# Performance work log

Hardware: AMD Instinct MI355X
Metric: run time of the kernel (lower is better)

## Reference

```python
import jax, jax.numpy as jnp
import numpy as np

PI = 3.141592653589793
L, B, D, EMAS = 4096, 16, 128, 8


def setup_inputs() -> dict:
    key = jax.random.key(0)
    x = jax.random.normal(key, (L, B, D), dtype=jnp.float32)
    # learned parameter of the EMA module: log-space decays
    log_decay = jnp.linspace(-PI, PI, EMAS, dtype=jnp.float32)
    return {"x": x, "log_decay": log_decay}


def reference(x, log_decay):
    # decay per EMA channel, in (0, 1)
    decay = jax.nn.sigmoid(log_decay)                     # [emas]
    # initial state: x[0] repeated along new emas axis
    state = jnp.broadcast_to(x[0][..., None], x[0].shape + (decay.shape[0],))  # [B, D, emas]

    def ema_step(ema_0, x_1):
        # x_1: [B, D, 1] broadcasts against decay [emas]
        ema_1 = decay * x_1 + (1.0 - decay) * ema_0
        return ema_1, ema_1

    _, ema_x = jax.lax.scan(ema_step, state, x[..., None])  # ys: [L, B, D, emas]
    return ema_x
```

## Files before the change

### kernel.cpp

```cpp
#include <hip/hip_runtime.h>


#define LL    4096
#define BB    16
#define DD    128
#define EMAS  8
#define BDSZ  (BB * DD)
#define CHUNK 32
#define HALO  128
#define NCHUNK (LL / CHUNK)
#define U     16

typedef float f32x4 __attribute__((ext_vector_type(4)));

__global__ __launch_bounds__(256) void ema_kernel(const float* __restrict__ x,
                                                  const float* __restrict__ log_decay,
                                                  float* __restrict__ out) {
    const int tid   = threadIdx.x;
    const int d     = tid & (DD - 1);
    const int bsub  = tid >> 7;
    const int bg    = blockIdx.x & 7;
    const int chunk = blockIdx.x >> 3;
    const int b     = bg * 2 + bsub;
    const int off   = b * DD + d;

    float dec[EMAS], a[EMAS];
#pragma unroll
    for (int e = 0; e < EMAS; ++e) {
        const float ld = log_decay[e];
        const float dd = 1.0f / (1.0f + __expf(-ld));
        dec[e] = dd;
        a[e]   = 1.0f - dd;
    }

    const int cstart = chunk * CHUNK;
    int l0 = cstart - HALO;
    if (l0 < 0) l0 = 0;
    const int nsteps   = (cstart - l0) + CHUNK;
    const int nblk     = nsteps / U;
    const int halo_blk = (cstart - l0) / U;

    const float* xb = x + (size_t)l0 * BDSZ + off;

    const float s0 = *xb;
    float s[EMAS];
#pragma unroll
    for (int e = 0; e < EMAS; ++e) s[e] = s0;

    f32x4* op = (f32x4*)(out + ((size_t)cstart * BDSZ + off) * EMAS);
    const int opstride = BDSZ * EMAS / 4;

#define LOADBLK(BUF, IDX)                                                      \
    do {                                                                       \
        int _i = (IDX); if (_i > nblk - 1) _i = nblk - 1;                      \
        const float* _p = xb + (size_t)_i * U * BDSZ;                          \
        _Pragma("unroll")                                                      \
        for (int u = 0; u < U; ++u) (BUF)[u] = _p[(size_t)u * BDSZ];           \
    } while (0)

#define PROCESS(BUF, J)                                                        \
    do {                                                                       \
        if ((J) >= halo_blk) {                                                 \
            _Pragma("unroll")                                                  \
            for (int u = 0; u < U; ++u) {                                      \
                const float xv = (BUF)[u];                                     \
                _Pragma("unroll")                                              \
                for (int e = 0; e < EMAS; ++e)                                 \
                    s[e] = fmaf(a[e], s[e], dec[e] * xv);                      \
                f32x4 lo = {s[0], s[1], s[2], s[3]};                           \
                f32x4 hi = {s[4], s[5], s[6], s[7]};                           \
                op[0] = lo;                                                    \
                op[1] = hi;                                                    \
                op += opstride;                                                \
            }                                                                  \
        } else {                                                               \
            _Pragma("unroll")                                                  \
            for (int u = 0; u < U; ++u) {                                      \
                const float xv = (BUF)[u];                                     \
                _Pragma("unroll")                                              \
                for (int e = 0; e < EMAS; ++e)                                 \
                    s[e] = fmaf(a[e], s[e], dec[e] * xv);                      \
            }                                                                  \
        }                                                                      \
    } while (0)

    float b0[U], b1[U], b2[U];
    LOADBLK(b0, 0);
    LOADBLK(b1, 1);

    int j = 0;
    for (; j + 2 < nblk; j += 3) {
        LOADBLK(b2, j + 2);
        PROCESS(b0, j);
        LOADBLK(b0, j + 3);
        PROCESS(b1, j + 1);
        LOADBLK(b1, j + 4);
        PROCESS(b2, j + 2);
    }
    if (j < nblk)     PROCESS(b0, j);
    if (j + 1 < nblk) PROCESS(b1, j + 1);
#undef PROCESS
#undef LOADBLK
}

extern "C" void kernel_launch(void* const* d_in, const int* in_sizes, int n_in,
                              void* d_out, int out_size, void* d_ws, size_t ws_size,
                              hipStream_t stream) {
    const float* x  = (const float*)d_in[0];
    const float* ld = (const float*)d_in[1];
    float* out      = (float*)d_out;
    (void)in_sizes; (void)n_in; (void)out_size; (void)d_ws; (void)ws_size;

    dim3 grid(NCHUNK * 8);
    dim3 block(256);
    ema_kernel<<<grid, block, 0, stream>>>(x, ld, out);
}
```

Baseline: 67.04 us.

## Prefetch chunk inputs upfront and split halo warmup from output loop

Switches to 1024-thread blocks covering half the batch-feature plane per chunk. The 32 output-step inputs are now loaded at kernel start alongside the halo prefetch, which overlaps their latency with the halo warmup. Halo processing uses smaller 8-step blocks with a separate pipelined loop, and the output phase runs without per-block branching. In exchange it raises register pressure, and the larger blocks reduce the number of workgroups.

Measured after the change: 104.6 us. +56.0%, slower.

```diff
diff --git a/kernel.cpp b/kernel.cpp
--- a/kernel.cpp
+++ b/kernel.cpp
@@ -9,20 +9,17 @@
 #define CHUNK 32
 #define HALO  128
 #define NCHUNK (LL / CHUNK)
-#define U     16
+#define U     8
 
 typedef float f32x4 __attribute__((ext_vector_type(4)));
 
-__global__ __launch_bounds__(256) void ema_kernel(const float* __restrict__ x,
-                                                  const float* __restrict__ log_decay,
-                                                  float* __restrict__ out) {
-    const int tid   = threadIdx.x;
-    const int d     = tid & (DD - 1);
-    const int bsub  = tid >> 7;
-    const int bg    = blockIdx.x & 7;
-    const int chunk = blockIdx.x >> 3;
-    const int b     = bg * 2 + bsub;
-    const int off   = b * DD + d;
+__global__ __launch_bounds__(1024) void ema_kernel(const float* __restrict__ x,
+                                                   const float* __restrict__ log_decay,
+                                                   float* __restrict__ out) {
+    const int tid  = threadIdx.x;
+    const int half = blockIdx.x & 1;
+    const int c    = blockIdx.x >> 1;
+    const int off  = (half << 10) + tid;
 
     float dec[EMAS], a[EMAS];
 #pragma unroll
@@ -33,74 +30,85 @@
         a[e]   = 1.0f - dd;
     }
 
-    const int cstart = chunk * CHUNK;
-    int l0 = cstart - HALO;
-    if (l0 < 0) l0 = 0;
-    const int nsteps   = (cstart - l0) + CHUNK;
-    const int nblk     = nsteps / U;
-    const int halo_blk = (cstart - l0) / U;
-
-    const float* xb = x + (size_t)l0 * BDSZ + off;
+    const int cstart = c * CHUNK;
+    const int front  = cstart < HALO ? cstart : HALO;
+    const int nfb    = front / U;
+    const float* xb  = x + (size_t)(cstart - front) * BDSZ + off;
 
     const float s0 = *xb;
     float s[EMAS];
 #pragma unroll
     for (int e = 0; e < EMAS; ++e) s[e] = s0;
 
-    f32x4* op = (f32x4*)(out + ((size_t)cstart * BDSZ + off) * EMAS);
-    const int opstride = BDSZ * EMAS / 4;
-
-#define LOADBLK(BUF, IDX)                                                      \
+#define LOADF(BUF, IDX)                                                        \
     do {                                                                       \
-        int _i = (IDX); if (_i > nblk - 1) _i = nblk - 1;                      \
-        const float* _p = xb + (size_t)_i * U * BDSZ;                          \
-        _Pragma("unroll")                                                      \
-        for (int u = 0; u < U; ++u) (BUF)[u] = _p[(size_t)u * BDSZ];           \
-    } while (0)
-
-#define PROCESS(BUF, J)                                                        \
-    do {                                                                       \
-        if ((J) >= halo_blk) {                                                 \
+        if ((IDX) < nfb) {                                                     \
+            const float* _p = xb + (size_t)(IDX) * U * BDSZ;                   \
             _Pragma("unroll")                                                  \
-            for (int u = 0; u < U; ++u) {                                      \
-                const float xv = (BUF)[u];                                     \
-                _Pragma("unroll")                                              \
-                for (int e = 0; e < EMAS; ++e)                                 \
-                    s[e] = fmaf(a[e], s[e], dec[e] * xv);                      \
-                f32x4 lo = {s[0], s[1], s[2], s[3]};                           \
-                f32x4 hi = {s[4], s[5], s[6], s[7]};                           \
-                op[0] = lo;                                                    \
-                op[1] = hi;                                                    \
-                op += opstride;                                                \
-            }                                                                  \
-        } else {                                                               \
-            _Pragma("unroll")                                                  \
-            for (int u = 0; u < U; ++u) {                                      \
-                const float xv = (BUF)[u];                                     \
-                _Pragma("unroll")                                              \
-                for (int e = 0; e < EMAS; ++e)                                 \
-                    s[e] = fmaf(a[e], s[e], dec[e] * xv);                      \
-            }                                                                  \
+            for (int u = 0; u < U; ++u) (BUF)[u] = _p[(size_t)u * BDSZ];       \
         }                                                                      \
     } while (0)
 
-    float b0[U], b1[U], b2[U];
-    LOADBLK(b0, 0);
-    LOADBLK(b1, 1);
+#define PROCF(BUF)                                                             \
+    do {                                                                       \
+        _Pragma("unroll")                                                      \
+        for (int u = 0; u < U; ++u) {                                          \
+            const float xv = (BUF)[u];                                         \
+            _Pragma("unroll")                                                  \
+            for (int e = 0; e < EMAS; ++e)                                     \
+                s[e] = fmaf(a[e], s[e], dec[e] * xv);                          \
+        }                                                                      \
+    } while (0)
+
+    float f0[U], f1[U], f2[U];
+    LOADF(f0, 0);
+    LOADF(f1, 1);
+
+    float c0[16], c1[16];
+    {
+        const float* xs = xb + (size_t)front * BDSZ;
+#pragma unroll
+        for (int u = 0; u < 16; ++u) c0[u] = xs[(size_t)u * BDSZ];
+#pragma unroll
+        for (int u = 0; u < 16; ++u) c1[u] = xs[(size_t)(16 + u) * BDSZ];
+    }
 
     int j = 0;
-    for (; j + 2 < nblk; j += 3) {
-        LOADBLK(b2, j + 2);
-        PROCESS(b0, j);
-        LOADBLK(b0, j + 3);
-        PROCESS(b1, j + 1);
-        LOADBLK(b1, j + 4);
-        PROCESS(b2, j + 2);
+    for (; j + 2 < nfb; j += 3) {
+        LOADF(f2, j + 2);
+        PROCF(f0);
+        LOADF(f0, j + 3);
+        PROCF(f1);
+        LOADF(f1, j + 4);
+        PROCF(f2);
     }
-    if (j < nblk)     PROCESS(b0, j);
-    if (j + 1 < nblk) PROCESS(b1, j + 1);
-#undef PROCESS
-#undef LOADBLK
+    if (j < nfb)     PROCF(f0);
+    if (j + 1 < nfb) PROCF(f1);
+
+    f32x4* op = (f32x4*)out + ((size_t)cstart * BDSZ + off) * 2;
+    const int opstride = BDSZ * EMAS / 4;
+
+#define PROCS(BUF)                                                             \
+    do {                                                                       \
+        _Pragma("unroll")                                                      \
+        for (int u = 0; u < 16; ++u) {                                         \
+            const float xv = (BUF)[u];                                         \
+            _Pragma("unroll")                                                  \
+            for (int e = 0; e < EMAS; ++e)                                     \
+                s[e] = fmaf(a[e], s[e], dec[e] * xv);                          \
+            f32x4 lo = {s[0], s[1], s[2], s[3]};                               \
+            f32x4 hi = {s[4], s[5], s[6], s[7]};                               \
+            op[0] = lo;                                                        \
+            op[1] = hi;                                                        \
+            op += opstride;                                                    \
+        }                                                                      \
+    } while (0)
+
+    PROCS(c0);
+    PROCS(c1);
+#undef PROCS
+#undef PROCF
+#undef LOADF
 }
 
 extern "C" void kernel_launch(void* const* d_in, const int* in_sizes, int n_in,
@@ -111,7 +119,7 @@
     float* out      = (float*)d_out;
     (void)in_sizes; (void)n_in; (void)out_size; (void)d_ws; (void)ws_size;
 
-    dim3 grid(NCHUNK * 8);
-    dim3 block(256);
+    dim3 grid(NCHUNK * 2);
+    dim3 block(1024);
     ema_kernel<<<grid, block, 0, stream>>>(x, ld, out);
 }
```
